# Optimization experiments

Hardware: AMD Instinct MI355X
Metric: run time of the kernel (lower is better)

## Reference

```python
import jax, jax.numpy as jnp
import numpy as np

D = 1024   # hidden_size
H = 16     # n_head
K = 64     # head_size
B = 4
T = 1024
LAYER_ID = 12
NUM_LAYERS = 24
D_MIX = 32
D_DECAY = 64


def setup_inputs() -> dict:
    key = jax.random.key(0)
    ks = jax.random.split(key, 12)
    r01 = LAYER_ID / (NUM_LAYERS - 1)          # ratio_0_to_1
    r10 = 1.0 - LAYER_ID / NUM_LAYERS          # ratio_1_to_almost0
    ddd = jnp.arange(D, dtype=jnp.float32) / D
    maa = lambda p: (1.0 - ddd ** p).reshape(1, 1, D)
    inp = {}
    inp['x'] = jax.random.normal(ks[0], (B, T, D), jnp.float32)
    inp['time_maa_x'] = maa(r10)
    inp['time_maa_w'] = maa(r10)
    inp['time_maa_k'] = maa(r10)
    inp['time_maa_v'] = (1.0 - (ddd ** r10 + 0.3 * r01)).reshape(1, 1, D)
    inp['time_maa_r'] = maa(0.5 * r10)
    inp['time_maa_g'] = maa(0.5 * r10)
    # torch inits time_maa_w1 to zeros (trivial); use small uniform like w2 for a non-degenerate test
    inp['time_maa_w1'] = jax.random.uniform(ks[1], (D, D_MIX * 5), jnp.float32, -0.01, 0.01)
    inp['time_maa_w2'] = jax.random.uniform(ks[2], (5, D_MIX, D), jnp.float32, -0.01, 0.01)
    n = jnp.arange(D, dtype=jnp.float32)
    inp['time_decay'] = (-6.0 + 5.0 * (n / (D - 1)) ** (0.7 + 1.3 * r01)).reshape(1, 1, D)
    inp['time_decay_w1'] = jax.random.uniform(ks[3], (D, D_DECAY), jnp.float32, -0.01, 0.01)
    inp['time_decay_w2'] = jax.random.uniform(ks[4], (D_DECAY, D), jnp.float32, -0.01, 0.01)
    for nm, kk in zip(['W_r', 'W_k', 'W_v', 'W_g', 'W_o'], ks[5:10]):
        inp[nm] = jax.random.normal(kk, (D, D), jnp.float32) * 0.02
    inp['ln_w'] = jnp.ones((D,), jnp.float32)
    inp['ln_b'] = jnp.zeros((D,), jnp.float32)
    return inp


def _bidir_shift(x):
    # (x[i-1] + x[i+1]) / 2 with zero padding at the boundaries
    left = jnp.pad(x[:, :-1, :], ((0, 0), (1, 0), (0, 0)))
    right = jnp.pad(x[:, 1:, :], ((0, 0), (0, 1), (0, 0)))
    return 0.5 * (left + right)


def _lion_attention(r, k, v, w):
    # r,k,v,w: (B,H,T,Khd), w = -exp(decay) <= 0
    Tn = r.shape[2]
    cs = jnp.cumsum(w, axis=2)
    cs_b = cs - w
    shift_f = cs[:, :, Tn // 2:Tn // 2 + 1, :]
    shift_b = cs_b[:, :, Tn // 2:Tn // 2 + 1, :]
    cf = jnp.clip(cs - shift_f, -60.0, 60.0)
    cb = jnp.clip(cs_b - shift_b, -60.0, 60.0)
    # A_fwd = tril(Q*e^{cf} @ (K*e^{-cf})^T); A_bwd = triu(Q*e^{-cb} @ (K*e^{cb})^T, 1)
    A_f = jnp.einsum('bhik,bhjk->bhij', r * jnp.exp(cf), k * jnp.exp(-cf))
    A_b = jnp.einsum('bhik,bhjk->bhij', r * jnp.exp(-cb), k * jnp.exp(cb))
    idx = jnp.arange(Tn)
    lower = idx[:, None] >= idx[None, :]   # tril incl. diagonal
    A = jnp.where(lower, A_f, A_b)         # == tril(A_f) + triu(A_b, 1)
    return jnp.einsum('bhij,bhjk->bhik', A, v)


def reference(x, time_maa_x, time_maa_w, time_maa_k, time_maa_v, time_maa_r, time_maa_g,
              time_maa_w1, time_maa_w2, time_decay, time_decay_w1, time_decay_w2,
              W_r, W_k, W_v, W_g, W_o, ln_w, ln_b):
    Bn, Tn, Dn = x.shape
    Hh, Kk = H, Dn // H
    dxprev = _bidir_shift(x) - x
    # data-dependent token-shift mixing coefficients (LoRA-style)
    xxx = jnp.tanh((x + dxprev * time_maa_x) @ time_maa_w1)          # (B,T,5*32)
    mm = jnp.einsum('btfm,fmd->fbtd', xxx.reshape(Bn, Tn, 5, D_MIX), time_maa_w2)
    mw, mk, mv, mr, mg = mm[0], mm[1], mm[2], mm[3], mm[4]
    xw = x + dxprev * (time_maa_w + mw)
    xk = x + dxprev * (time_maa_k + mk)
    xv = x + dxprev * (time_maa_v + mv)
    xr = x + dxprev * (time_maa_r + mr)
    xg = x + dxprev * (time_maa_g + mg)
    r = xr @ W_r.T
    k = xk @ W_k.T
    v = xv @ W_v.T
    g = jax.nn.silu(xg @ W_g.T)
    w = time_decay + jnp.tanh(xw @ time_decay_w1) @ time_decay_w2   # (B,T,D)
    to_h = lambda t: t.reshape(Bn, Tn, Hh, Kk).transpose(0, 2, 1, 3)
    y = _lion_attention(to_h(r), to_h(k), to_h(v), -jnp.exp(to_h(w)))
    y = y.transpose(0, 2, 1, 3).reshape(Bn * Tn, Dn)
    # GroupNorm(n_head groups, eps = 1e-5 * head_size_divisor^2)
    eps = 1e-5 * 64.0
    yg = y.reshape(Bn * Tn, Hh, Kk)
    mu = jnp.mean(yg, axis=-1, keepdims=True)
    var = jnp.var(yg, axis=-1, keepdims=True)
    yn = ((yg - mu) * jax.lax.rsqrt(var + eps)).reshape(Bn * Tn, Dn) * ln_w + ln_b
    y = yn.reshape(Bn, Tn, Dn)
    return (y * g) @ W_o.T
```

## Files before the change

### kernel.cpp

```cpp
#include <hip/hip_runtime.h>
#include <math.h>

#define NB 4
#define TT 1024
#define DD 1024
#define NTOK 4096
#define ND (NTOK*DD)

typedef __attribute__((ext_vector_type(8))) short bh8;
typedef __attribute__((ext_vector_type(4))) float fx4;

__device__ __forceinline__ unsigned short f2bf(float f) {
    unsigned int b = __float_as_uint(f);
    b += 0x7fffu + ((b >> 16) & 1u);
    return (unsigned short)(b >> 16);
}

__device__ __forceinline__ unsigned pkbf(float a, float b) {
#if __has_builtin(__builtin_amdgcn_cvt_pk_bf16_f32)
    auto r = __builtin_amdgcn_cvt_pk_bf16_f32(a, b);
    unsigned u;
    __builtin_memcpy(&u, &r, 4);
    return u;
#else
    return ((unsigned)f2bf(b) << 16) | f2bf(a);
#endif
}

#define GLD16(gp, lp) __builtin_amdgcn_global_load_lds( \
    (__attribute__((address_space(1))) void*)(gp), \
    (__attribute__((address_space(3))) void*)(lp), 16, 0, 0)

#define BARF() do { __builtin_amdgcn_s_barrier(); asm volatile("" ::: "memory"); } while (0)

__global__ __launch_bounds__(256) void k_prep(const float* __restrict__ W_r, const float* __restrict__ W_k,
                                              const float* __restrict__ W_v, const float* __restrict__ W_g,
                                              const float* __restrict__ W_o,
                                              const float* __restrict__ w1, const float* __restrict__ dw1,
                                              const float* __restrict__ w2,
                                              unsigned short* __restrict__ Wrb, unsigned short* __restrict__ Wkb,
                                              unsigned short* __restrict__ Wvb, unsigned short* __restrict__ Wgb,
                                              unsigned short* __restrict__ Wob,
                                              unsigned short* __restrict__ w1T, unsigned short* __restrict__ dw1T,
                                              unsigned short* __restrict__ w2T16) {
    int y = blockIdx.y, bx = blockIdx.x, tid = threadIdx.x;
    if (y < 5) {
        if (bx >= 512) return;
        const float* s = (y == 0) ? W_r : (y == 1) ? W_k : (y == 2) ? W_v : (y == 3) ? W_g : W_o;
        unsigned short* d = (y == 0) ? Wrb : (y == 1) ? Wkb : (y == 2) ? Wvb : (y == 3) ? Wgb : Wob;
        int i = (bx * 256 + tid) * 8;
        float4 a = *(const float4*)(s + i);
        float4 b = *(const float4*)(s + i + 4);
        uint4 o;
        o.x = pkbf(a.x, a.y);
        o.y = pkbf(a.z, a.w);
        o.z = pkbf(b.x, b.y);
        o.w = pkbf(b.z, b.w);
        *(uint4*)(d + i) = o;
    } else if (y == 5) {
        int o = bx * 256 + tid;
        int r = o & 1023, c = o >> 10;
        w1T[o] = f2bf(w1[r * 160 + c]);
    } else {
        if (bx < 256) {
            int o = bx * 256 + tid;
            int r = o & 1023, c = o >> 10;
            dw1T[o] = f2bf(dw1[r * 64 + c]);
        } else if (bx < 276) {
            int wi = bx - 256;
            int f = wi >> 2;
            int d = (wi & 3) * 256 + tid;
#pragma unroll 8
            for (int m = 0; m < 32; m++)
                w2T16[(size_t)(f * 1024 + d) * 32 + m] = f2bf(w2[(size_t)(f * 32 + m) * 1024 + d]);
        }
    }
}

__global__ __launch_bounds__(256) void k_mixx(const float* __restrict__ x,
                                              const float* __restrict__ maa_x,
                                              unsigned short* __restrict__ xmix16,
                                              float* __restrict__ dxf) {
    int base = (blockIdx.x * 256 + threadIdx.x) * 4;
    int t = (base >> 10) & 1023;
    int d = base & 1023;
    float4 xv = *(const float4*)(x + base);
    float4 xm = (t > 0)    ? *(const float4*)(x + base - 1024) : make_float4(0, 0, 0, 0);
    float4 xp = (t < 1023) ? *(const float4*)(x + base + 1024) : make_float4(0, 0, 0, 0);
    float4 ma = *(const float4*)(maa_x + d);
    float dx0 = 0.5f * (xm.x + xp.x) - xv.x;
    float dx1 = 0.5f * (xm.y + xp.y) - xv.y;
    float dx2 = 0.5f * (xm.z + xp.z) - xv.z;
    float dx3 = 0.5f * (xm.w + xp.w) - xv.w;
    uint2 o;
    o.x = pkbf(xv.x + dx0 * ma.x, xv.y + dx1 * ma.y);
    o.y = pkbf(xv.z + dx2 * ma.z, xv.w + dx3 * ma.w);
    *(uint2*)(xmix16 + base) = o;
    float4 dq; dq.x = dx0; dq.y = dx1; dq.z = dx2; dq.w = dx3;
    *(float4*)(dxf + base) = dq;
}

__global__ __launch_bounds__(256) void k_xxx2(const unsigned short* __restrict__ xmix16,
                                              const unsigned short* __restrict__ w1T,
                                              unsigned short* __restrict__ xxx16) {
    __shared__ __align__(16) float red[4][10][64][4];
    int tid = threadIdx.x;
    int lane = tid & 63, wv = tid >> 6;
    int l15 = lane & 15, qd = lane >> 4;
    int m0 = blockIdx.x * 16;
    fx4 acc[10];
#pragma unroll
    for (int nt = 0; nt < 10; nt++)
#pragma unroll
        for (int r = 0; r < 4; r++) acc[nt][r] = 0.f;
    int kb0 = wv * 256;
#pragma unroll 2
    for (int kb = kb0; kb < kb0 + 256; kb += 32) {
        bh8 af = *(const bh8*)(xmix16 + (size_t)(m0 + l15) * 1024 + kb + qd * 8);
#pragma unroll
        for (int nt = 0; nt < 10; nt++) {
            bh8 bf = *(const bh8*)(w1T + (size_t)(nt * 16 + l15) * 1024 + kb + qd * 8);
            acc[nt] = __builtin_amdgcn_mfma_f32_16x16x32_bf16(af, bf, acc[nt], 0, 0, 0);
        }
    }
#pragma unroll
    for (int nt = 0; nt < 10; nt++)
        *(fx4*)&red[wv][nt][lane][0] = acc[nt];
    __syncthreads();
    if (wv == 0) {
#pragma unroll
        for (int nt = 0; nt < 10; nt++) {
            fx4 s = *(const fx4*)&red[0][nt][lane][0];
            s = s + *(const fx4*)&red[1][nt][lane][0];
            s = s + *(const fx4*)&red[2][nt][lane][0];
            s = s + *(const fx4*)&red[3][nt][lane][0];
#pragma unroll
            for (int r = 0; r < 4; r++)
                xxx16[(size_t)(m0 + qd * 4 + r) * 160 + nt * 16 + l15] = f2bf(tanhf(s[r]));
        }
    }
}

__global__ __launch_bounds__(256, 2) void k_mmix(const float* __restrict__ x,
                                                 const float* __restrict__ dxf,
                                                 const unsigned short* __restrict__ xxx16,
                                                 const unsigned short* __restrict__ w2T16,
                                                 const float* __restrict__ maa_w,
                                                 const float* __restrict__ maa_k,
                                                 const float* __restrict__ maa_v,
                                                 const float* __restrict__ maa_r,
                                                 const float* __restrict__ maa_g,
                                                 unsigned short* __restrict__ xw16,
                                                 unsigned short* __restrict__ xk16,
                                                 unsigned short* __restrict__ xv16,
                                                 unsigned short* __restrict__ xr16,
                                                 unsigned short* __restrict__ xg16) {
    int tid = threadIdx.x;
    int w = tid >> 6, lane = tid & 63, l15 = lane & 15, qd = lane >> 4;
    int n0 = blockIdx.x * 64;
    int m0w = blockIdx.y * 128 + w * 32;
    const float* maap[5] = {maa_w, maa_k, maa_v, maa_r, maa_g};
    unsigned short* outp[5] = {xw16, xk16, xv16, xr16, xg16};
    float xin[8][4], dxv[8][4];
#pragma unroll
    for (int mi = 0; mi < 2; mi++)
#pragma unroll
        for (int r = 0; r < 4; r++) {
            int tok = m0w + mi * 16 + qd * 4 + r;
#pragma unroll
            for (int ni = 0; ni < 4; ni++) {
                int d = n0 + ni * 16 + l15;
                size_t idx = (size_t)tok * 1024 + d;
                xin[mi * 4 + r][ni] = x[idx];
                dxv[mi * 4 + r][ni] = dxf[idx];
            }
        }
#pragma unroll
    for (int f = 0; f < 5; f++) {
        bh8 af[2], bf[4];
#pragma unroll
        for (int mi = 0; mi < 2; mi++)
            af[mi] = *(const bh8*)(xxx16 + (size_t)(m0w + mi * 16 + l15) * 160 + f * 32 + qd * 8);
#pragma unroll
        for (int ni = 0; ni < 4; ni++)
            bf[ni] = *(const bh8*)(w2T16 + (size_t)(f * 1024 + n0 + ni * 16 + l15) * 32 + qd * 8);
        fx4 acc[2][4];
#pragma unroll
        for (int mi = 0; mi < 2; mi++)
#pragma unroll
            for (int ni = 0; ni < 4; ni++) {
#pragma unroll
                for (int r = 0; r < 4; r++) acc[mi][ni][r] = 0.f;
                acc[mi][ni] = __builtin_amdgcn_mfma_f32_16x16x32_bf16(af[mi], bf[ni], acc[mi][ni], 0, 0, 0);
            }
        const float* maa = maap[f];
        unsigned short* op = outp[f];
#pragma unroll
        for (int ni = 0; ni < 4; ni++) {
            float mv = maa[n0 + ni * 16 + l15];
#pragma unroll
            for (int mi = 0; mi < 2; mi++)
#pragma unroll
                for (int r = 0; r < 4; r++) {
                    float o = xin[mi * 4 + r][ni] + dxv[mi * 4 + r][ni] * (mv + acc[mi][ni][r]);
                    op[(size_t)(m0w + mi * 16 + qd * 4 + r) * 1024 + n0 + ni * 16 + l15] = f2bf(o);
                }
        }
    }
}

__global__ __launch_bounds__(256) void k_dec1m(const unsigned short* __restrict__ xw16,
                                               const unsigned short* __restrict__ dw1T,
                                               float* __restrict__ dech) {
    __shared__ __align__(16) float red[4][4][64][4];
    int tid = threadIdx.x;
    int lane = tid & 63, wv = tid >> 6;
    int l15 = lane & 15, qd = lane >> 4;
    int m0 = blockIdx.x * 16;
    fx4 acc[4];
#pragma unroll
    for (int nt = 0; nt < 4; nt++)
#pragma unroll
        for (int r = 0; r < 4; r++) acc[nt][r] = 0.f;
    int kb0 = wv * 256;
#pragma unroll 2
    for (int kb = kb0; kb < kb0 + 256; kb += 32) {
        bh8 af = *(const bh8*)(xw16 + (size_t)(m0 + l15) * 1024 + kb + qd * 8);
#pragma unroll
        for (int nt = 0; nt < 4; nt++) {
            bh8 bf = *(const bh8*)(dw1T + (size_t)(nt * 16 + l15) * 1024 + kb + qd * 8);
            acc[nt] = __builtin_amdgcn_mfma_f32_16x16x32_bf16(af, bf, acc[nt], 0, 0, 0);
        }
    }
#pragma unroll
    for (int nt = 0; nt < 4; nt++)
        *(fx4*)&red[wv][nt][lane][0] = acc[nt];
    __syncthreads();
    if (wv == 0) {
#pragma unroll
        for (int nt = 0; nt < 4; nt++) {
            fx4 s = *(const fx4*)&red[0][nt][lane][0];
            s = s + *(const fx4*)&red[1][nt][lane][0];
            s = s + *(const fx4*)&red[2][nt][lane][0];
            s = s + *(const fx4*)&red[3][nt][lane][0];
#pragma unroll
            for (int r = 0; r < 4; r++)
                dech[(size_t)(m0 + qd * 4 + r) * 64 + nt * 16 + l15] = tanhf(s[r]);
        }
    }
}

__global__ __launch_bounds__(256) void k_dec2(const float* __restrict__ dech,
                                              const float* __restrict__ dw2,
                                              const float* __restrict__ tdec,
                                              float* __restrict__ ew) {
    __shared__ float hl[8][64];
    int tid = threadIdx.x;
    int tok0 = blockIdx.x * 8;
    {
        int l = tid;        hl[l >> 6][l & 63] = dech[tok0 * 64 + l];
        l = tid + 256;      hl[l >> 6][l & 63] = dech[tok0 * 64 + l];
    }
    __syncthreads();
#pragma unroll 1
    for (int c = 0; c < 4; c++) {
        int d = c * 256 + tid;
        float acc[8] = {};
#pragma unroll 8
        for (int j = 0; j < 64; j++) {
            float wv = dw2[j * 1024 + d];
#pragma unroll
            for (int g = 0; g < 8; g++) acc[g] = fmaf(hl[g][j], wv, acc[g]);
        }
        float td = tdec[d];
#pragma unroll
        for (int g = 0; g < 8; g++) ew[(tok0 + g) * 1024 + d] = -expf(td + acc[g]);
    }
}

__global__ __launch_bounds__(64) void k_scan1(const float* __restrict__ ew, float* __restrict__ segsum) {
    int bx = blockIdx.x;
    int b = bx >> 9, seg = (bx >> 4) & 31, dch = bx & 15;
    int d = dch * 64 + threadIdx.x;
    size_t base = ((size_t)(b * 1024 + seg * 32)) * 1024 + d;
    float s = 0.f;
#pragma unroll 8
    for (int t = 0; t < 32; t++) s += ew[base + (size_t)t * 1024];
    segsum[(b * 32 + seg) * 1024 + d] = s;
}

__global__ __launch_bounds__(64) void k_scan3(const float* __restrict__ ew, const float* __restrict__ segsum,
                                              float* __restrict__ cf, float* __restrict__ cb) {
    int bx = blockIdx.x;
    int b = bx >> 9, seg = (bx >> 4) & 31, dch = bx & 15;
    int d = dch * 64 + threadIdx.x;
    float run = 0.f, pre = 0.f, off16 = 0.f;
#pragma unroll
    for (int s = 0; s < 32; s++) {
        float tv = segsum[(b * 32 + s) * 1024 + d];
        if (s == seg) pre = run;
        if (s == 16) off16 = run;
        run += tv;
    }
    float e512 = ew[((size_t)(b * 1024 + 512)) * 1024 + d];
    float sb = off16;
    float sf = off16 + e512;
    float cum = pre;
    size_t base = ((size_t)(b * 1024 + seg * 32)) * 1024 + d;
#pragma unroll 4
    for (int t = 0; t < 32; t++) {
        float prev = cum;
        cum += ew[base + (size_t)t * 1024];
        cf[base + (size_t)t * 1024] = fminf(fmaxf(cum - sf, -60.f), 60.f);
        cb[base + (size_t)t * 1024] = fminf(fmaxf(prev - sb, -60.f), 60.f);
    }
}

template<int NW, int BNv>
__device__ __forceinline__ void gemm_v5(const unsigned short* __restrict__ A,
                                        const unsigned short* __restrict__ W,
                                        int m0, int n0, int mode,
                                        float* __restrict__ Cf,
                                        unsigned short* __restrict__ O1,
                                        unsigned short* __restrict__ O2,
                                        const float* __restrict__ cfp,
                                        const float* __restrict__ cbp,
                                        char* smem) {
    constexpr int AR = 128 / NW;
    constexpr int AG = AR / 16;
    constexpr int BR = BNv / NW;
    constexpr int BG = BR / 16;
    constexpr int LPW = AG + BG;
    constexpr int SLOT = (128 + BNv) * 64;
    constexpr int WNC = BNv / 64;

    int tid = threadIdx.x;
    int lane = tid & 63, w = tid >> 6;
    int l15 = lane & 15, qd = lane >> 4;
    int wm = w / WNC, wn = w % WNC;
    int lr = lane >> 2, lb = lane & 3;
    int gblk = lb ^ ((lr >> 1) & 3);
    const unsigned short* aSrc = A + (size_t)(m0 + w * AR + lr) * 1024 + gblk * 8;
    const unsigned short* bSrc = W + (size_t)(n0 + w * BR + lr) * 1024 + gblk * 8;
    int rc = (qd ^ ((l15 >> 1) & 3)) * 8;
    int arow = (wm * 64 + l15) * 32 + rc;
    int brow = (wn * 64 + l15) * 32 + rc;

    auto stage = [&](int off, int kbv) {
        unsigned short* _sa = (unsigned short*)(smem + off);
        unsigned short* _sb = _sa + 128 * 32;
#pragma unroll
        for (int i = 0; i < AG; ++i)
            GLD16(aSrc + kbv + (size_t)i * 16 * 1024, _sa + (w * AR + i * 16) * 32);
#pragma unroll
        for (int i = 0; i < BG; ++i)
            GLD16(bSrc + kbv + (size_t)i * 16 * 1024, _sb + (w * BR + i * 16) * 32);
    };

    fx4 acc[4][4];
#pragma unroll
    for (int mt = 0; mt < 4; mt++)
#pragma unroll
        for (int nt = 0; nt < 4; nt++)
#pragma unroll
            for (int r = 0; r < 4; r++) acc[mt][nt][r] = 0.f;

    stage(0, 0);
    stage(SLOT, 32);
    if constexpr (LPW == 3) asm volatile("s_waitcnt vmcnt(3)" ::: "memory");
    else                    asm volatile("s_waitcnt vmcnt(4)" ::: "memory");
    BARF();

    int oc = 0, on = SLOT, o2 = 2 * SLOT;
#pragma unroll 1
    for (int t = 0; t < 32; ++t) {
        if (t < 30) stage(o2, (t + 2) * 32);
        const unsigned short* cA = (const unsigned short*)(smem + oc);
        const unsigned short* cB = cA + 128 * 32;
        bh8 a[4], b[4];
#pragma unroll
        for (int mt = 0; mt < 4; ++mt) a[mt] = *(const bh8*)(cA + arow + mt * 512);
#pragma unroll
        for (int nt = 0; nt < 4; ++nt) b[nt] = *(const bh8*)(cB + brow + nt * 512);
        __builtin_amdgcn_s_setprio(1);
#pragma unroll
        for (int nt = 0; nt < 4; ++nt)
#pragma unroll
            for (int mt = 0; mt < 4; ++mt)
                acc[mt][nt] = __builtin_amdgcn_mfma_f32_16x16x32_bf16(a[mt], b[nt], acc[mt][nt], 0, 0, 0);
        __builtin_amdgcn_s_setprio(0);
        asm volatile("s_waitcnt lgkmcnt(0)" ::: "memory");
        if (t < 30) {
            if constexpr (LPW == 3) asm volatile("s_waitcnt vmcnt(3)" ::: "memory");
            else                    asm volatile("s_waitcnt vmcnt(4)" ::: "memory");
        } else if (t == 30) {
            asm volatile("s_waitcnt vmcnt(0)" ::: "memory");
        }
        BARF();
        int tmp = oc; oc = on; on = o2; o2 = tmp;
    }

    int mb = m0 + wm * 64, nb = n0 + wn * 64;
    if (mode <= 1) {
#pragma unroll
        for (int mt = 0; mt < 4; mt++)
#pragma unroll
            for (int nt = 0; nt < 4; nt++)
#pragma unroll
                for (int r = 0; r < 4; r++) {
                    float v = acc[mt][nt][r];
                    if (mode == 1) v = v / (1.f + __expf(-v));
                    Cf[(size_t)(mb + mt * 16 + qd * 4 + r) * 1024 + nb + nt * 16 + l15] = v;
                }
    } else if (mode <= 3) {
        float s1 = (mode == 2) ? 1.f : -1.f;
#pragma unroll
        for (int mt = 0; mt < 4; mt++)
#pragma unroll
            for (int nt = 0; nt < 4; nt++)
#pragma unroll
                for (int r = 0; r < 4; r++) {
                    size_t idx = (size_t)(mb + mt * 16 + qd * 4 + r) * 1024 + nb + nt * 16 + l15;
                    float v = acc[mt][nt][r];
                    O1[idx] = f2bf(v * __expf(s1 * cfp[idx]));
                    O2[idx] = f2bf(v * __expf(-s1 * cbp[idx]));
                }
    } else {
        unsigned short* T = (unsigned short*)smem;
        int bq = m0 >> 10, t0 = m0 & 1023;
#pragma unroll
        for (int mt = 0; mt < 4; mt++)
#pragma unroll
            for (int nt = 0; nt < 4; nt++) {
                int dl = wn * 64 + nt * 16 + l15;
                int tl = wm * 64 + mt * 16 + qd * 4;
                uint2 pk2;
                pk2.x = pkbf(acc[mt][nt][0], acc[mt][nt][1]);
                pk2.y = pkbf(acc[mt][nt][2], acc[mt][nt][3]);
                *(uint2*)(T + dl * 136 + tl) = pk2;
            }
        asm volatile("s_waitcnt lgkmcnt(0)" ::: "memory");
        BARF();
#pragma unroll
        for (int p = 0; p < 8; ++p) {
            int idx = p * (NW * 64) + tid;
            int dd = idx >> 4, u = idx & 15;
            uint4 vv = *(const uint4*)(T + dd * 136 + u * 8);
            *(uint4*)(O1 + (size_t)(bq * 1024 + n0 + dd) * 1024 + t0 + u * 8) = vv;
        }
    }
}

__global__ __launch_bounds__(512, 4) void k_qkvg(const unsigned short* __restrict__ xr16,
                                                 const unsigned short* __restrict__ xk16,
                                                 const unsigned short* __restrict__ xv16,
                                                 const unsigned short* __restrict__ xg16,
                                                 const unsigned short* __restrict__ Wrb,
                                                 const unsigned short* __restrict__ Wkb,
                                                 const unsigned short* __restrict__ Wvb,
                                                 const unsigned short* __restrict__ Wgb,
                                                 unsigned short* __restrict__ qf, unsigned short* __restrict__ qb,
                                                 unsigned short* __restrict__ kf, unsigned short* __restrict__ kb,
                                                 unsigned short* __restrict__ vvt,
                                                 float* __restrict__ gg,
                                                 const float* __restrict__ cf, const float* __restrict__ cb) {
    __shared__ __align__(16) char smem[73728];
    int flat = blockIdx.x;
    int wkid = (flat & 7) * 64 + (flat >> 3);
    int gy = wkid >> 7;
    int rem = wkid & 127;
    int m0 = (rem >> 2) * 128, n0 = (rem & 3) * 256;
    const unsigned short* Ap = (gy == 0) ? xr16 : (gy == 1) ? xk16 : (gy == 2) ? xv16 : xg16;
    const unsigned short* Wp = (gy == 0) ? Wrb : (gy == 1) ? Wkb : (gy == 2) ? Wvb : Wgb;
    int mode = (gy == 0) ? 2 : (gy == 1) ? 3 : (gy == 2) ? 4 : 1;
    unsigned short* o1 = (gy == 0) ? qf : (gy == 1) ? kf : (gy == 2) ? vvt : nullptr;
    unsigned short* o2 = (gy == 0) ? qb : (gy == 1) ? kb : nullptr;
    float* cfo = (gy == 3) ? gg : nullptr;
    gemm_v5<8, 256>(Ap, Wp, m0, n0, mode, cfo, o1, o2, cf, cb, smem);
}

__global__ __launch_bounds__(256, 3) void k_gemmo(const unsigned short* __restrict__ z16,
                                                  const unsigned short* __restrict__ Wob,
                                                  float* __restrict__ out) {
    __shared__ __align__(16) char smem[49152];
    int flat = blockIdx.x;
    int wkid = (flat & 7) * 32 + (flat >> 3);
    int m0 = (wkid >> 3) * 128, n0 = (wkid & 7) * 128;
    gemm_v5<4, 128>(z16, Wob, m0, n0, 0, out, nullptr, nullptr, nullptr, nullptr, smem);
}

__global__ __launch_bounds__(256, 2) void k_attn(const unsigned short* __restrict__ qf,
                                                 const unsigned short* __restrict__ qb,
                                                 const unsigned short* __restrict__ kf,
                                                 const unsigned short* __restrict__ kb,
                                                 const unsigned short* __restrict__ vvt,
                                                 float* __restrict__ y) {
    __shared__ __align__(16) char smem[32768];
    unsigned short* sK = (unsigned short*)smem;
    unsigned short* sV = (unsigned short*)(smem + 16384);
    int tid = threadIdx.x;
    int w = tid >> 6, lane = tid & 63, l15 = lane & 15, qd = lane >> 4;
    int bid = blockIdx.x;
    int bh = (bid & 7) + ((bid >> 6) << 3);
    int ib = (bid >> 3) & 7;
    int b = bh >> 4, h = bh & 15;
    int i0w = ib * 128 + w * 32;
    int bt0 = b * 1024;
    const unsigned short* vrow = vvt + (size_t)(b * 1024 + h * 64 + w * 16 + l15) * 1024 + qd * 8;
    int fmax = (i0w + 31) >> 6;
    int bmin = i0w >> 6;
    int srcA = l15 + ((lane & 16) << 1);
    int srcB = srcA + 16;
    fx4 yacc[4][2];
#pragma unroll
    for (int mt = 0; mt < 4; mt++)
#pragma unroll
        for (int nt = 0; nt < 2; nt++)
#pragma unroll
            for (int r = 0; r < 4; r++) yacc[mt][nt][r] = 0.f;

    for (int phase = 0; phase < 2; phase++) {
        const unsigned short* Q = phase ? qb : qf;
        const unsigned short* K = phase ? kb : kf;
        bh8 qfr[2][2];
#pragma unroll
        for (int nt = 0; nt < 2; nt++)
#pragma unroll
            for (int ks = 0; ks < 2; ks++)
                qfr[nt][ks] = *(const bh8*)(Q + (size_t)(bt0 + i0w + nt * 16 + l15) * 1024
                                              + h * 64 + ks * 32 + qd * 8);
        int jlo = phase == 0 ? 0 : 2 * ib;
        int jhi = phase == 0 ? 2 * ib + 1 : 15;
        const unsigned short* krow = K + (size_t)(bt0 + w * 16 + l15) * 1024 + h * 64 + qd * 8;
        for (int jt2 = jlo; jt2 <= jhi; jt2 += 2) {
            __syncthreads();
#pragma unroll
            for (int u = 0; u < 2; ++u) {
                size_t jb = (size_t)(jt2 + u) * 64;
                GLD16(krow + jb * 1024,        sK + u * 4096 + w * 512);
                GLD16(krow + jb * 1024 + 32,   sK + u * 4096 + 2048 + w * 512);
                GLD16(vrow + jb,               sV + u * 4096 + w * 512);
                GLD16(vrow + jb + 32,          sV + u * 4096 + 2048 + w * 512);
            }
            __syncthreads();
#pragma unroll
            for (int u = 0; u < 2; ++u) {
                int jt = jt2 + u;
                int jb = jt * 64;
                const unsigned short* bK = sK + u * 4096;
                const unsigned short* bV = sV + u * 4096;
                bool active = (phase == 0) ? (jt <= fmax) : (jt >= bmin);
                if (!active) continue;
                bool needmask = (phase == 0) ? (jb + 63 > i0w) : (i0w + 31 >= jb);
                bh8 kc[8];
#pragma unroll
                for (int fi = 0; fi < 8; fi++)
                    kc[fi] = *(const bh8*)(bK + fi * 512 + lane * 8);
                fx4 sacc[4][2];
#pragma unroll
                for (int mt = 0; mt < 4; mt++)
#pragma unroll
                    for (int nt = 0; nt < 2; nt++)
#pragma unroll
                        for (int r = 0; r < 4; r++) sacc[mt][nt][r] = 0.f;
#pragma unroll
                for (int ks = 0; ks < 2; ks++)
#pragma unroll
                    for (int mt = 0; mt < 4; mt++)
#pragma unroll
                        for (int nt = 0; nt < 2; nt++)
                            sacc[mt][nt] = __builtin_amdgcn_mfma_f32_16x16x32_bf16(kc[ks * 4 + mt], qfr[nt][ks], sacc[mt][nt], 0, 0, 0);
                uint2 pk[4][2];
#pragma unroll
                for (int mt = 0; mt < 4; mt++)
#pragma unroll
                    for (int nt = 0; nt < 2; nt++) {
                        fx4 s = sacc[mt][nt];
                        if (needmask) {
                            int ii = i0w + nt * 16 + l15;
                            int jj0 = jb + mt * 16 + qd * 4;
#pragma unroll
                            for (int r = 0; r < 4; r++) {
                                bool keep = (phase == 0) ? (ii >= jj0 + r) : (ii < jj0 + r);
                                if (!keep) s[r] = 0.f;
                            }
                        }
                        pk[mt][nt].x = pkbf(s[0], s[1]);
                        pk[mt][nt].y = pkbf(s[2], s[3]);
                    }
                bh8 vc[8];
#pragma unroll
                for (int fi = 0; fi < 8; fi++)
                    vc[fi] = *(const bh8*)(bV + fi * 512 + lane * 8);
#pragma unroll
                for (int ks2 = 0; ks2 < 2; ks2++) {
#pragma unroll
                    for (int nt = 0; nt < 2; nt++) {
                        int lox  = __shfl((int)pk[2 * ks2][nt].x,     srcA);
                        int hix  = __shfl((int)pk[2 * ks2 + 1][nt].x, srcA);
                        int loy  = __shfl((int)pk[2 * ks2][nt].y,     srcA);
                        int hiy  = __shfl((int)pk[2 * ks2 + 1][nt].y, srcA);
                        int lox2 = __shfl((int)pk[2 * ks2][nt].x,     srcB);
                        int hix2 = __shfl((int)pk[2 * ks2 + 1][nt].x, srcB);
                        int loy2 = __shfl((int)pk[2 * ks2][nt].y,     srcB);
                        int hiy2 = __shfl((int)pk[2 * ks2 + 1][nt].y, srcB);
                        union { int4 i; bh8 h; } cv;
                        cv.i.x = (qd & 2) ? hix  : lox;
                        cv.i.y = (qd & 2) ? hiy  : loy;
                        cv.i.z = (qd & 2) ? hix2 : lox2;
                        cv.i.w = (qd & 2) ? hiy2 : loy2;
#pragma unroll
                        for (int mt = 0; mt < 4; mt++)
                            yacc[mt][nt] = __builtin_amdgcn_mfma_f32_16x16x32_bf16(vc[ks2 * 4 + mt], cv.h, yacc[mt][nt], 0, 0, 0);
                    }
                }
            }
        }
    }
#pragma unroll
    for (int mt = 0; mt < 4; mt++)
#pragma unroll
        for (int nt = 0; nt < 2; nt++) {
            fx4 s = yacc[mt][nt];
            float4 o; o.x = s[0]; o.y = s[1]; o.z = s[2]; o.w = s[3];
            *(float4*)&y[(size_t)(bt0 + i0w + nt * 16 + l15) * 1024 + h * 64 + mt * 16 + qd * 4] = o;
        }
}

__global__ __launch_bounds__(256) void k_gn(const float* __restrict__ y,
                                            const float* __restrict__ g,
                                            const float* __restrict__ lnw,
                                            const float* __restrict__ lnb,
                                            unsigned short* __restrict__ z16) {
    int tid = threadIdx.x;
    int lane = tid & 63;
    int wv = tid >> 6;
    int group = blockIdx.x * 4 + wv;
    int tok = group >> 4, h = group & 15;
    int d = h * 64 + lane;
    size_t idx = (size_t)tok * 1024 + d;
    float val = y[idx];
    float s = val, s2 = val * val;
#pragma unroll
    for (int off = 32; off > 0; off >>= 1) {
        s  += __shfl_xor(s, off, 64);
        s2 += __shfl_xor(s2, off, 64);
    }
    float mu = s * (1.f / 64.f);
    float var = s2 * (1.f / 64.f) - mu * mu;
    float inv = rsqrtf(var + 6.4e-4f);
    float yn = (val - mu) * inv * lnw[d] + lnb[d];
    z16[idx] = f2bf(yn * g[idx]);
}

extern "C" void kernel_launch(void* const* d_in, const int* in_sizes, int n_in,
                              void* d_out, int out_size, void* d_ws, size_t ws_size,
                              hipStream_t stream) {
    const float* x     = (const float*)d_in[0];
    const float* maa_x = (const float*)d_in[1];
    const float* maa_w = (const float*)d_in[2];
    const float* maa_k = (const float*)d_in[3];
    const float* maa_v = (const float*)d_in[4];
    const float* maa_r = (const float*)d_in[5];
    const float* maa_g = (const float*)d_in[6];
    const float* w1    = (const float*)d_in[7];
    const float* w2    = (const float*)d_in[8];
    const float* tdec  = (const float*)d_in[9];
    const float* dw1   = (const float*)d_in[10];
    const float* dw2   = (const float*)d_in[11];
    const float* W_r   = (const float*)d_in[12];
    const float* W_k   = (const float*)d_in[13];
    const float* W_v   = (const float*)d_in[14];
    const float* W_g   = (const float*)d_in[15];
    const float* W_o   = (const float*)d_in[16];
    const float* lnw   = (const float*)d_in[17];
    const float* lnb   = (const float*)d_in[18];

    float* ws = (float*)d_ws;
    size_t o = 0;
    float* dech   = ws + o; o += 262144;
    float* segsum = ws + o; o += 131072;
    float* ew     = ws + o; o += 4194304;
    float* cf     = ws + o; o += 4194304;
    float* cb     = ws + o; o += 4194304;
    float* gg     = ws + o; o += 4194304;
    unsigned short* us = (unsigned short*)(ws + o);
    size_t u = 0;
    unsigned short* xmix16 = us + u; u += 4194304;
    unsigned short* xw16 = us + u; u += 4194304;
    unsigned short* xr16 = us + u; u += 4194304;
    unsigned short* xk16 = us + u; u += 4194304;
    unsigned short* xv16 = us + u; u += 4194304;
    unsigned short* xg16 = us + u; u += 4194304;
    unsigned short* qf   = us + u; u += 4194304;
    unsigned short* qb   = us + u; u += 4194304;
    unsigned short* kf   = us + u; u += 4194304;
    unsigned short* kb   = us + u; u += 4194304;
    unsigned short* vvt  = us + u; u += 4194304;
    unsigned short* Wrb  = us + u; u += 1048576;
    unsigned short* Wkb  = us + u; u += 1048576;
    unsigned short* Wvb  = us + u; u += 1048576;
    unsigned short* Wgb  = us + u; u += 1048576;
    unsigned short* Wob  = us + u; u += 1048576;
    unsigned short* w1T  = us + u; u += 163840;
    unsigned short* dw1T = us + u; u += 65536;
    unsigned short* xxx16 = us + u; u += 655360;
    unsigned short* w2T16 = us + u; u += 163840;
    float* yb0 = cf;
    unsigned short* z16 = xr16;
    float* dxf = gg;

    k_prep<<<dim3(640, 7), 256, 0, stream>>>(W_r, W_k, W_v, W_g, W_o, w1, dw1, w2,
                                             Wrb, Wkb, Wvb, Wgb, Wob, w1T, dw1T, w2T16);
    k_mixx<<<4096, 256, 0, stream>>>(x, maa_x, xmix16, dxf);
    k_xxx2<<<256, 256, 0, stream>>>(xmix16, w1T, xxx16);
    k_mmix<<<dim3(16, 32), 256, 0, stream>>>(x, dxf, xxx16, w2T16, maa_w, maa_k, maa_v, maa_r, maa_g,
                                             xw16, xk16, xv16, xr16, xg16);
    k_dec1m<<<256, 256, 0, stream>>>(xw16, dw1T, dech);
    k_dec2<<<512, 256, 0, stream>>>(dech, dw2, tdec, ew);
    k_scan1<<<2048, 64, 0, stream>>>(ew, segsum);
    k_scan3<<<2048, 64, 0, stream>>>(ew, segsum, cf, cb);
    k_qkvg<<<dim3(512), dim3(512), 0, stream>>>(xr16, xk16, xv16, xg16, Wrb, Wkb, Wvb, Wgb,
                                                qf, qb, kf, kb, vvt, gg, cf, cb);
    k_attn<<<512, 256, 0, stream>>>(qf, qb, kf, kb, vvt, yb0);
    k_gn<<<16384, 256, 0, stream>>>(yb0, gg, lnw, lnb, z16);
    k_gemmo<<<256, 256, 0, stream>>>(z16, Wob, (float*)d_out);
}
```

Measured before the change: 338.0 us.

## Recompute shift delta in mmix and load attention K/V directly from global

Stops writing the fp32 shift-delta buffer in the mix kernel. The mmix kernel now recomputes it from neighbouring rows of x, which removes a 16MB write and its later read but adds two extra x loads per element. In the attention kernel, the LDS staging of K/V tiles and the barriers are dropped. Each wave now loads MFMA operands straight from global memory, with s_setprio raised around the MFMA blocks and occupancy launch bounds relaxed. Wave-level redundant global loads replace shared reuse, so performance leans on cache hits.

```diff
diff --git a/kernel.cpp b/kernel.cpp
--- a/kernel.cpp
+++ b/kernel.cpp
@@ -79,8 +79,7 @@
 
 __global__ __launch_bounds__(256) void k_mixx(const float* __restrict__ x,
                                               const float* __restrict__ maa_x,
-                                              unsigned short* __restrict__ xmix16,
-                                              float* __restrict__ dxf) {
+                                              unsigned short* __restrict__ xmix16) {
     int base = (blockIdx.x * 256 + threadIdx.x) * 4;
     int t = (base >> 10) & 1023;
     int d = base & 1023;
@@ -88,16 +87,14 @@
     float4 xm = (t > 0)    ? *(const float4*)(x + base - 1024) : make_float4(0, 0, 0, 0);
     float4 xp = (t < 1023) ? *(const float4*)(x + base + 1024) : make_float4(0, 0, 0, 0);
     float4 ma = *(const float4*)(maa_x + d);
-    float dx0 = 0.5f * (xm.x + xp.x) - xv.x;
-    float dx1 = 0.5f * (xm.y + xp.y) - xv.y;
-    float dx2 = 0.5f * (xm.z + xp.z) - xv.z;
-    float dx3 = 0.5f * (xm.w + xp.w) - xv.w;
     uint2 o;
-    o.x = pkbf(xv.x + dx0 * ma.x, xv.y + dx1 * ma.y);
-    o.y = pkbf(xv.z + dx2 * ma.z, xv.w + dx3 * ma.w);
+    float a0 = xv.x + (0.5f * (xm.x + xp.x) - xv.x) * ma.x;
+    float a1 = xv.y + (0.5f * (xm.y + xp.y) - xv.y) * ma.y;
+    float a2 = xv.z + (0.5f * (xm.z + xp.z) - xv.z) * ma.z;
+    float a3 = xv.w + (0.5f * (xm.w + xp.w) - xv.w) * ma.w;
+    o.x = pkbf(a0, a1);
+    o.y = pkbf(a2, a3);
     *(uint2*)(xmix16 + base) = o;
-    float4 dq; dq.x = dx0; dq.y = dx1; dq.z = dx2; dq.w = dx3;
-    *(float4*)(dxf + base) = dq;
 }
 
 __global__ __launch_bounds__(256) void k_xxx2(const unsigned short* __restrict__ xmix16,
@@ -142,7 +139,6 @@
 }
 
 __global__ __launch_bounds__(256, 2) void k_mmix(const float* __restrict__ x,
-                                                 const float* __restrict__ dxf,
                                                  const unsigned short* __restrict__ xxx16,
                                                  const unsigned short* __restrict__ w2T16,
                                                  const float* __restrict__ maa_w,
@@ -167,12 +163,16 @@
 #pragma unroll
         for (int r = 0; r < 4; r++) {
             int tok = m0w + mi * 16 + qd * 4 + r;
+            int t = tok & 1023;
 #pragma unroll
             for (int ni = 0; ni < 4; ni++) {
                 int d = n0 + ni * 16 + l15;
                 size_t idx = (size_t)tok * 1024 + d;
-                xin[mi * 4 + r][ni] = x[idx];
-                dxv[mi * 4 + r][ni] = dxf[idx];
+                float xv = x[idx];
+                float xm1 = (t > 0)    ? x[idx - 1024] : 0.f;
+                float xp1 = (t < 1023) ? x[idx + 1024] : 0.f;
+                xin[mi * 4 + r][ni] = xv;
+                dxv[mi * 4 + r][ni] = 0.5f * (xm1 + xp1) - xv;
             }
         }
 #pragma unroll
@@ -489,15 +489,12 @@
     gemm_v5<4, 128>(z16, Wob, m0, n0, 0, out, nullptr, nullptr, nullptr, nullptr, smem);
 }
 
-__global__ __launch_bounds__(256, 2) void k_attn(const unsigned short* __restrict__ qf,
-                                                 const unsigned short* __restrict__ qb,
-                                                 const unsigned short* __restrict__ kf,
-                                                 const unsigned short* __restrict__ kb,
-                                                 const unsigned short* __restrict__ vvt,
-                                                 float* __restrict__ y) {
-    __shared__ __align__(16) char smem[32768];
-    unsigned short* sK = (unsigned short*)smem;
-    unsigned short* sV = (unsigned short*)(smem + 16384);
+__global__ __launch_bounds__(256) void k_attn(const unsigned short* __restrict__ qf,
+                                              const unsigned short* __restrict__ qb,
+                                              const unsigned short* __restrict__ kf,
+                                              const unsigned short* __restrict__ kb,
+                                              const unsigned short* __restrict__ vvt,
+                                              float* __restrict__ y) {
     int tid = threadIdx.x;
     int w = tid >> 6, lane = tid & 63, l15 = lane & 15, qd = lane >> 4;
     int bid = blockIdx.x;
@@ -506,11 +503,11 @@
     int b = bh >> 4, h = bh & 15;
     int i0w = ib * 128 + w * 32;
     int bt0 = b * 1024;
-    const unsigned short* vrow = vvt + (size_t)(b * 1024 + h * 64 + w * 16 + l15) * 1024 + qd * 8;
     int fmax = (i0w + 31) >> 6;
     int bmin = i0w >> 6;
     int srcA = l15 + ((lane & 16) << 1);
     int srcB = srcA + 16;
+    const unsigned short* vB = vvt + (size_t)(b * 1024 + h * 64 + l15) * 1024 + qd * 8;
     fx4 yacc[4][2];
 #pragma unroll
     for (int mt = 0; mt < 4; mt++)
@@ -529,90 +526,80 @@
             for (int ks = 0; ks < 2; ks++)
                 qfr[nt][ks] = *(const bh8*)(Q + (size_t)(bt0 + i0w + nt * 16 + l15) * 1024
                                               + h * 64 + ks * 32 + qd * 8);
-        int jlo = phase == 0 ? 0 : 2 * ib;
-        int jhi = phase == 0 ? 2 * ib + 1 : 15;
-        const unsigned short* krow = K + (size_t)(bt0 + w * 16 + l15) * 1024 + h * 64 + qd * 8;
-        for (int jt2 = jlo; jt2 <= jhi; jt2 += 2) {
-            __syncthreads();
-#pragma unroll
-            for (int u = 0; u < 2; ++u) {
-                size_t jb = (size_t)(jt2 + u) * 64;
-                GLD16(krow + jb * 1024,        sK + u * 4096 + w * 512);
-                GLD16(krow + jb * 1024 + 32,   sK + u * 4096 + 2048 + w * 512);
-                GLD16(vrow + jb,               sV + u * 4096 + w * 512);
-                GLD16(vrow + jb + 32,          sV + u * 4096 + 2048 + w * 512);
-            }
-            __syncthreads();
-#pragma unroll
-            for (int u = 0; u < 2; ++u) {
-                int jt = jt2 + u;
-                int jb = jt * 64;
-                const unsigned short* bK = sK + u * 4096;
-                const unsigned short* bV = sV + u * 4096;
-                bool active = (phase == 0) ? (jt <= fmax) : (jt >= bmin);
-                if (!active) continue;
-                bool needmask = (phase == 0) ? (jb + 63 > i0w) : (i0w + 31 >= jb);
-                bh8 kc[8];
-#pragma unroll
-                for (int fi = 0; fi < 8; fi++)
-                    kc[fi] = *(const bh8*)(bK + fi * 512 + lane * 8);
-                fx4 sacc[4][2];
+        const unsigned short* kB = K + (size_t)(bt0 + l15) * 1024 + h * 64 + qd * 8;
+        int lo = phase == 0 ? 0 : bmin;
+        int hi = phase == 0 ? fmax : 15;
+        for (int jt = lo; jt <= hi; jt++) {
+            int jb = jt * 64;
+            bool needmask = (phase == 0) ? (jb + 63 > i0w) : (i0w + 31 >= jb);
+            bh8 kc[8];
+#pragma unroll
+            for (int ks = 0; ks < 2; ks++)
 #pragma unroll
                 for (int mt = 0; mt < 4; mt++)
+                    kc[ks * 4 + mt] = *(const bh8*)(kB + (size_t)(jb + mt * 16) * 1024 + ks * 32);
+            fx4 sacc[4][2];
+#pragma unroll
+            for (int mt = 0; mt < 4; mt++)
+#pragma unroll
+                for (int nt = 0; nt < 2; nt++)
+#pragma unroll
+                    for (int r = 0; r < 4; r++) sacc[mt][nt][r] = 0.f;
+            __builtin_amdgcn_s_setprio(1);
+#pragma unroll
+            for (int ks = 0; ks < 2; ks++)
+#pragma unroll
+                for (int mt = 0; mt < 4; mt++)
 #pragma unroll
                     for (int nt = 0; nt < 2; nt++)
-#pragma unroll
-                        for (int r = 0; r < 4; r++) sacc[mt][nt][r] = 0.f;
-#pragma unroll
-                for (int ks = 0; ks < 2; ks++)
+                        sacc[mt][nt] = __builtin_amdgcn_mfma_f32_16x16x32_bf16(kc[ks * 4 + mt], qfr[nt][ks], sacc[mt][nt], 0, 0, 0);
+            __builtin_amdgcn_s_setprio(0);
+            bh8 vc[8];
+#pragma unroll
+            for (int ks2 = 0; ks2 < 2; ks2++)
+#pragma unroll
+                for (int mt = 0; mt < 4; mt++)
+                    vc[ks2 * 4 + mt] = *(const bh8*)(vB + (size_t)(mt * 16) * 1024 + jb + ks2 * 32);
+            uint2 pk[4][2];
+#pragma unroll
+            for (int mt = 0; mt < 4; mt++)
+#pragma unroll
+                for (int nt = 0; nt < 2; nt++) {
+                    fx4 s = sacc[mt][nt];
+                    if (needmask) {
+                        int ii = i0w + nt * 16 + l15;
+                        int jj0 = jb + mt * 16 + qd * 4;
+#pragma unroll
+                        for (int r = 0; r < 4; r++) {
+                            bool keep = (phase == 0) ? (ii >= jj0 + r) : (ii < jj0 + r);
+                            if (!keep) s[r] = 0.f;
+                        }
+                    }
+                    pk[mt][nt].x = pkbf(s[0], s[1]);
+                    pk[mt][nt].y = pkbf(s[2], s[3]);
+                }
+#pragma unroll
+            for (int ks2 = 0; ks2 < 2; ks2++) {
+#pragma unroll
+                for (int nt = 0; nt < 2; nt++) {
+                    int lox  = __shfl((int)pk[2 * ks2][nt].x,     srcA);
+                    int hix  = __shfl((int)pk[2 * ks2 + 1][nt].x, srcA);
+                    int loy  = __shfl((int)pk[2 * ks2][nt].y,     srcA);
+                    int hiy  = __shfl((int)pk[2 * ks2 + 1][nt].y, srcA);
+                    int lox2 = __shfl((int)pk[2 * ks2][nt].x,     srcB);
+                    int hix2 = __shfl((int)pk[2 * ks2 + 1][nt].x, srcB);
+                    int loy2 = __shfl((int)pk[2 * ks2][nt].y,     srcB);
+                    int hiy2 = __shfl((int)pk[2 * ks2 + 1][nt].y, srcB);
+                    union { int4 i; bh8 h; } cv;
+                    cv.i.x = (qd & 2) ? hix  : lox;
+                    cv.i.y = (qd & 2) ? hiy  : loy;
+                    cv.i.z = (qd & 2) ? hix2 : lox2;
+                    cv.i.w = (qd & 2) ? hiy2 : loy2;
+                    __builtin_amdgcn_s_setprio(1);
 #pragma unroll
                     for (int mt = 0; mt < 4; mt++)
-#pragma unroll
-                        for (int nt = 0; nt < 2; nt++)
-                            sacc[mt][nt] = __builtin_amdgcn_mfma_f32_16x16x32_bf16(kc[ks * 4 + mt], qfr[nt][ks], sacc[mt][nt], 0, 0, 0);
-                uint2 pk[4][2];
-#pragma unroll
-                for (int mt = 0; mt < 4; mt++)
-#pragma unroll
-                    for (int nt = 0; nt < 2; nt++) {
-                        fx4 s = sacc[mt][nt];
-                        if (needmask) {
-                            int ii = i0w + nt * 16 + l15;
-                            int jj0 = jb + mt * 16 + qd * 4;
-#pragma unroll
-                            for (int r = 0; r < 4; r++) {
-                                bool keep = (phase == 0) ? (ii >= jj0 + r) : (ii < jj0 + r);
-                                if (!keep) s[r] = 0.f;
-                            }
-                        }
-                        pk[mt][nt].x = pkbf(s[0], s[1]);
-                        pk[mt][nt].y = pkbf(s[2], s[3]);
-                    }
-                bh8 vc[8];
-#pragma unroll
-                for (int fi = 0; fi < 8; fi++)
-                    vc[fi] = *(const bh8*)(bV + fi * 512 + lane * 8);
-#pragma unroll
-                for (int ks2 = 0; ks2 < 2; ks2++) {
-#pragma unroll
-                    for (int nt = 0; nt < 2; nt++) {
-                        int lox  = __shfl((int)pk[2 * ks2][nt].x,     srcA);
-                        int hix  = __shfl((int)pk[2 * ks2 + 1][nt].x, srcA);
-                        int loy  = __shfl((int)pk[2 * ks2][nt].y,     srcA);
-                        int hiy  = __shfl((int)pk[2 * ks2 + 1][nt].y, srcA);
-                        int lox2 = __shfl((int)pk[2 * ks2][nt].x,     srcB);
-                        int hix2 = __shfl((int)pk[2 * ks2 + 1][nt].x, srcB);
-                        int loy2 = __shfl((int)pk[2 * ks2][nt].y,     srcB);
-                        int hiy2 = __shfl((int)pk[2 * ks2 + 1][nt].y, srcB);
-                        union { int4 i; bh8 h; } cv;
-                        cv.i.x = (qd & 2) ? hix  : lox;
-                        cv.i.y = (qd & 2) ? hiy  : loy;
-                        cv.i.z = (qd & 2) ? hix2 : lox2;
-                        cv.i.w = (qd & 2) ? hiy2 : loy2;
-#pragma unroll
-                        for (int mt = 0; mt < 4; mt++)
-                            yacc[mt][nt] = __builtin_amdgcn_mfma_f32_16x16x32_bf16(vc[ks2 * 4 + mt], cv.h, yacc[mt][nt], 0, 0, 0);
-                    }
+                        yacc[mt][nt] = __builtin_amdgcn_mfma_f32_16x16x32_bf16(vc[ks2 * 4 + mt], cv.h, yacc[mt][nt], 0, 0, 0);
+                    __builtin_amdgcn_s_setprio(0);
                 }
             }
         }
@@ -708,13 +695,12 @@
     unsigned short* w2T16 = us + u; u += 163840;
     float* yb0 = cf;
     unsigned short* z16 = xr16;
-    float* dxf = gg;
 
     k_prep<<<dim3(640, 7), 256, 0, stream>>>(W_r, W_k, W_v, W_g, W_o, w1, dw1, w2,
                                              Wrb, Wkb, Wvb, Wgb, Wob, w1T, dw1T, w2T16);
-    k_mixx<<<4096, 256, 0, stream>>>(x, maa_x, xmix16, dxf);
+    k_mixx<<<4096, 256, 0, stream>>>(x, maa_x, xmix16);
     k_xxx2<<<256, 256, 0, stream>>>(xmix16, w1T, xxx16);
-    k_mmix<<<dim3(16, 32), 256, 0, stream>>>(x, dxf, xxx16, w2T16, maa_w, maa_k, maa_v, maa_r, maa_g,
+    k_mmix<<<dim3(16, 32), 256, 0, stream>>>(x, xxx16, w2T16, maa_w, maa_k, maa_v, maa_r, maa_g,
                                              xw16, xk16, xv16, xr16, xg16);
     k_dec1m<<<256, 256, 0, stream>>>(xw16, dw1T, dech);
     k_dec2<<<512, 256, 0, stream>>>(dech, dw2, tdec, ew);
```

Result: slower. 355.9 us (+5.3%).
